# Optimization experiments

Measured on AMD Instinct MI355X. Metric: run time of the kernel, lower is better.

## Reference

```python
import jax, jax.numpy as jnp
import numpy as np

B, S, D = 4, 4096, 2048


def _xavier(key, d):
    bound = (6.0 / (d + d)) ** 0.5
    return jax.random.uniform(key, (d, d), jnp.float32, -bound, bound)


def setup_inputs() -> dict:
    key = jax.random.key(0)
    ks = jax.random.split(key, 7)
    return {
        "x": jax.random.normal(ks[0], (B, S, D), jnp.float32),
        "Wr": _xavier(ks[1], D),
        "Ww": _xavier(ks[2], D),
        "Wk": _xavier(ks[3], D),
        "Wv": _xavier(ks[4], D),
        "Wo": _xavier(ks[5], D),
        "time_decay": jax.random.uniform(ks[6], (D,), jnp.float32, -1.0, 0.0),
    }


def reference(x, Wr, Ww, Wk, Wv, Wo, time_decay):
    # Projections (torch nn.Linear computes x @ W.T)
    r = jax.nn.sigmoid(jnp.einsum("bsd,ed->bse", x, Wr))
    w = -jnp.exp(jnp.einsum("bsd,ed->bse", x, Ww))
    k = jnp.einsum("bsd,ed->bse", x, Wk)
    v = jnp.einsum("bsd,ed->bse", x, Wv)
    ewk = jnp.exp(w + k)                       # [B,S,D]
    decay = jnp.exp(time_decay)                # [D], per-channel decay

    def step(carry, inp):
        num, den = carry                       # each [B,D]
        ewk_t, v_t, r_t = inp                  # each [B,D]
        # t==0 with zero state reduces to ewk*v / ewk, matching torch branch
        num = decay * num + ewk_t * v_t
        den = decay * den + ewk_t
        wkv = num / (den + 1e-8)
        return (num, den), r_t * wkv

    init = (jnp.zeros((B, D), x.dtype), jnp.zeros((B, D), x.dtype))
    xs = (jnp.swapaxes(ewk, 0, 1), jnp.swapaxes(v, 0, 1), jnp.swapaxes(r, 0, 1))
    (num, den), ys = jax.lax.scan(step, init, xs)          # ys: [S,B,D]
    out = jnp.einsum("bsd,ed->bse", jnp.swapaxes(ys, 0, 1), Wo)
    final_state = jnp.stack([num, den], axis=1)            # [B,2,D]
    return out, final_state
```

## Files before the change

kernel.cpp:

```cpp
#include <hip/hip_runtime.h>
#include <cstdint>
#include <cstddef>


typedef unsigned short u16;
typedef __attribute__((ext_vector_type(8))) __bf16 bf16x8;
typedef __attribute__((ext_vector_type(4))) float f32x4;

#define AS1 __attribute__((address_space(1)))
#define AS3 __attribute__((address_space(3)))

static constexpr int BATCH  = 4;
static constexpr int SEQ    = 4096;
static constexpr int DIM    = 2048;
static constexpr int MROWS  = BATCH * SEQ;
static constexpr int NCHUNK = 128;
static constexpr int CLEN   = SEQ / NCHUNK;

__device__ __forceinline__ u16 f2bf(float f) {
    uint32_t u = __float_as_uint(f);
    u += 0x7fffu + ((u >> 16) & 1u);
    return (u16)(u >> 16);
}
__device__ __forceinline__ float bfl(uint32_t w) { return __uint_as_float(w << 16); }
__device__ __forceinline__ float bfh(uint32_t w) { return __uint_as_float(w & 0xffff0000u); }
__device__ __forceinline__ void unpack8(uint4 u, float* f) {
    f[0] = bfl(u.x); f[1] = bfh(u.x); f[2] = bfl(u.y); f[3] = bfh(u.y);
    f[4] = bfl(u.z); f[5] = bfh(u.z); f[6] = bfl(u.w); f[7] = bfh(u.w);
}
__device__ __forceinline__ uint32_t pack2(float a, float b) {
    return (uint32_t)f2bf(a) | ((uint32_t)f2bf(b) << 16);
}

__global__ void __launch_bounds__(256) cvt_kernel(const float* __restrict__ in, u16* __restrict__ out) {
    size_t i = ((size_t)blockIdx.x * blockDim.x + threadIdx.x) * 4;
    float4 f = *(const float4*)(in + i);
    u16 o0 = f2bf(f.x), o1 = f2bf(f.y), o2 = f2bf(f.z), o3 = f2bf(f.w);
    uint2 p = { (uint32_t)o0 | ((uint32_t)o1 << 16), (uint32_t)o2 | ((uint32_t)o3 << 16) };
    *(uint2*)(out + i) = p;
}

template<int EPI>
__global__ void __launch_bounds__(256, 2)
gemm_nt(const u16* __restrict__ A, const u16* __restrict__ Bw,
        float* __restrict__ Cf, u16* __restrict__ Cb) {
    __shared__ __align__(16) u16 As[128 * 32];
    __shared__ __align__(16) u16 Bs[128 * 32];
    const int tid  = threadIdx.x;
    const int lane = tid & 63;
    const int wv   = tid >> 6;
    const int wr   = (wv >> 1) * 64;
    const int wc   = (wv & 1) * 64;
    const int m0   = blockIdx.x * 128;
    const int n0   = blockIdx.y * 128;
    const int fr   = lane & 15;
    const int kg   = (lane >> 4) * 8;
    const int srow = tid >> 2;
    const int skc  = (tid & 3) * 8;

    f32x4 acc[4][4] = {};
    const size_t a_base = (size_t)(m0 + srow) * DIM + skc;
    const size_t b_base = (size_t)(n0 + srow) * DIM + skc;

    for (int k0 = 0; k0 < DIM; k0 += 32) {
        __builtin_amdgcn_global_load_lds((AS1 void*)(A + a_base + k0),
                                         (AS3 void*)(As + tid * 8), 16, 0, 0);
        __builtin_amdgcn_global_load_lds((AS1 void*)(A + a_base + (size_t)64 * DIM + k0),
                                         (AS3 void*)(As + (tid + 256) * 8), 16, 0, 0);
        __builtin_amdgcn_global_load_lds((AS1 void*)(Bw + b_base + k0),
                                         (AS3 void*)(Bs + tid * 8), 16, 0, 0);
        __builtin_amdgcn_global_load_lds((AS1 void*)(Bw + b_base + (size_t)64 * DIM + k0),
                                         (AS3 void*)(Bs + (tid + 256) * 8), 16, 0, 0);
        __syncthreads();
        bf16x8 af[4], bfr[4];
#pragma unroll
        for (int i = 0; i < 4; ++i)
            af[i] = *(const bf16x8*)(As + (wr + i * 16 + fr) * 32 + kg);
#pragma unroll
        for (int j = 0; j < 4; ++j)
            bfr[j] = *(const bf16x8*)(Bs + (wc + j * 16 + fr) * 32 + kg);
#pragma unroll
        for (int i = 0; i < 4; ++i)
#pragma unroll
            for (int j = 0; j < 4; ++j)
                acc[i][j] = __builtin_amdgcn_mfma_f32_16x16x32_bf16(af[i], bfr[j], acc[i][j], 0, 0, 0);
        __syncthreads();
    }

    const int rb_ = (lane >> 4) * 4;
#pragma unroll
    for (int i = 0; i < 4; ++i) {
#pragma unroll
        for (int j = 0; j < 4; ++j) {
#pragma unroll
            for (int rg = 0; rg < 4; ++rg) {
                const int row = m0 + wr + i * 16 + rb_ + rg;
                const int col = n0 + wc + j * 16 + fr;
                const float val = acc[i][j][rg];
                if (EPI == 0) {
                    Cf[(size_t)row * DIM + col] = val;
                } else if (EPI == 1) {
                    Cb[(size_t)row * DIM + col] = f2bf(1.0f / (1.0f + expf(-val)));
                } else {
                    Cb[(size_t)row * DIM + col] = f2bf(val);
                }
            }
        }
    }
}

__global__ void __launch_bounds__(256, 2)
gemm_ewk(const u16* __restrict__ A, const u16* __restrict__ Wk,
         const u16* __restrict__ Ww, u16* __restrict__ E) {
    __shared__ __align__(16) u16 As[128 * 32];
    __shared__ __align__(16) u16 Ks[128 * 32];
    __shared__ __align__(16) u16 Ws[128 * 32];
    const int tid  = threadIdx.x;
    const int lane = tid & 63;
    const int wv   = tid >> 6;
    const int wr   = (wv >> 1) * 64;
    const int wc   = (wv & 1) * 64;
    const int m0   = blockIdx.x * 128;
    const int n0   = blockIdx.y * 128;
    const int fr   = lane & 15;
    const int kg   = (lane >> 4) * 8;
    const int srow = tid >> 2;
    const int skc  = (tid & 3) * 8;

    f32x4 acck[4][4] = {};
    f32x4 accw[4][4] = {};
    const size_t a_base = (size_t)(m0 + srow) * DIM + skc;
    const size_t b_base = (size_t)(n0 + srow) * DIM + skc;

    for (int k0 = 0; k0 < DIM; k0 += 32) {
        __builtin_amdgcn_global_load_lds((AS1 void*)(A + a_base + k0),
                                         (AS3 void*)(As + tid * 8), 16, 0, 0);
        __builtin_amdgcn_global_load_lds((AS1 void*)(A + a_base + (size_t)64 * DIM + k0),
                                         (AS3 void*)(As + (tid + 256) * 8), 16, 0, 0);
        __builtin_amdgcn_global_load_lds((AS1 void*)(Wk + b_base + k0),
                                         (AS3 void*)(Ks + tid * 8), 16, 0, 0);
        __builtin_amdgcn_global_load_lds((AS1 void*)(Wk + b_base + (size_t)64 * DIM + k0),
                                         (AS3 void*)(Ks + (tid + 256) * 8), 16, 0, 0);
        __builtin_amdgcn_global_load_lds((AS1 void*)(Ww + b_base + k0),
                                         (AS3 void*)(Ws + tid * 8), 16, 0, 0);
        __builtin_amdgcn_global_load_lds((AS1 void*)(Ww + b_base + (size_t)64 * DIM + k0),
                                         (AS3 void*)(Ws + (tid + 256) * 8), 16, 0, 0);
        __syncthreads();
        bf16x8 af[4], kf[4], wf[4];
#pragma unroll
        for (int i = 0; i < 4; ++i)
            af[i] = *(const bf16x8*)(As + (wr + i * 16 + fr) * 32 + kg);
#pragma unroll
        for (int j = 0; j < 4; ++j) {
            kf[j] = *(const bf16x8*)(Ks + (wc + j * 16 + fr) * 32 + kg);
            wf[j] = *(const bf16x8*)(Ws + (wc + j * 16 + fr) * 32 + kg);
        }
#pragma unroll
        for (int i = 0; i < 4; ++i)
#pragma unroll
            for (int j = 0; j < 4; ++j) {
                acck[i][j] = __builtin_amdgcn_mfma_f32_16x16x32_bf16(af[i], kf[j], acck[i][j], 0, 0, 0);
                accw[i][j] = __builtin_amdgcn_mfma_f32_16x16x32_bf16(af[i], wf[j], accw[i][j], 0, 0, 0);
            }
        __syncthreads();
    }

    const int rb_ = (lane >> 4) * 4;
#pragma unroll
    for (int i = 0; i < 4; ++i)
#pragma unroll
        for (int j = 0; j < 4; ++j)
#pragma unroll
            for (int rg = 0; rg < 4; ++rg) {
                const int row = m0 + wr + i * 16 + rb_ + rg;
                const int col = n0 + wc + j * 16 + fr;
                const float e = expf(acck[i][j][rg] - expf(accw[i][j][rg]));
                E[(size_t)row * DIM + col] = f2bf(e);
            }
}

__global__ void __launch_bounds__(256)
scan_carry(const u16* __restrict__ ewk, const u16* __restrict__ v,
           const float* __restrict__ td,
           float* __restrict__ carN, float* __restrict__ carD) {
    const int b  = blockIdx.x / NCHUNK;
    const int c  = blockIdx.x % NCHUNK;
    const int d0 = threadIdx.x * 8;
    float dec[8], num[8], den[8];
#pragma unroll
    for (int z = 0; z < 8; ++z) { dec[z] = expf(td[d0 + z]); num[z] = 0.f; den[z] = 0.f; }
    const size_t base = ((size_t)b * SEQ + (size_t)c * CLEN) * DIM + d0;
    for (int t = 0; t < CLEN; ++t) {
        uint4 eu = *(const uint4*)(ewk + base + (size_t)t * DIM);
        uint4 vu = *(const uint4*)(v   + base + (size_t)t * DIM);
        float e[8], vv[8];
        unpack8(eu, e); unpack8(vu, vv);
#pragma unroll
        for (int z = 0; z < 8; ++z) {
            num[z] = dec[z] * num[z] + e[z] * vv[z];
            den[z] = dec[z] * den[z] + e[z];
        }
    }
    const size_t cb = ((size_t)(b * NCHUNK + c)) * DIM + d0;
    *(float4*)(carN + cb)     = { num[0], num[1], num[2], num[3] };
    *(float4*)(carN + cb + 4) = { num[4], num[5], num[6], num[7] };
    *(float4*)(carD + cb)     = { den[0], den[1], den[2], den[3] };
    *(float4*)(carD + cb + 4) = { den[4], den[5], den[6], den[7] };
}

__global__ void __launch_bounds__(256)
scan_combine(const float* __restrict__ carN, const float* __restrict__ carD,
             const float* __restrict__ td,
             float* __restrict__ stN, float* __restrict__ stD,
             float* __restrict__ fs) {
    const int i = blockIdx.x * 256 + threadIdx.x;
    const int b = i >> 11;
    const int d = i & (DIM - 1);
    const float decL = expf(td[d] * (float)CLEN);
    float num = 0.f, den = 0.f;
    for (int c = 0; c < NCHUNK; ++c) {
        const size_t idx = ((size_t)(b * NCHUNK + c)) * DIM + d;
        stN[idx] = num; stD[idx] = den;
        num = decL * num + carN[idx];
        den = decL * den + carD[idx];
    }
    fs[(size_t)b * 2 * DIM + d]       = num;
    fs[(size_t)b * 2 * DIM + DIM + d] = den;
}

__global__ void __launch_bounds__(256)
scan_apply(const u16* __restrict__ ewk, const u16* __restrict__ v,
           const u16* __restrict__ r, const float* __restrict__ td,
           const float* __restrict__ stN, const float* __restrict__ stD,
           u16* __restrict__ y) {
    const int b  = blockIdx.x / NCHUNK;
    const int c  = blockIdx.x % NCHUNK;
    const int d0 = threadIdx.x * 8;
    float dec[8], num[8], den[8];
    const size_t sb = ((size_t)(b * NCHUNK + c)) * DIM + d0;
    {
        float4 n0_ = *(const float4*)(stN + sb), n1_ = *(const float4*)(stN + sb + 4);
        float4 e0_ = *(const float4*)(stD + sb), e1_ = *(const float4*)(stD + sb + 4);
        num[0]=n0_.x; num[1]=n0_.y; num[2]=n0_.z; num[3]=n0_.w;
        num[4]=n1_.x; num[5]=n1_.y; num[6]=n1_.z; num[7]=n1_.w;
        den[0]=e0_.x; den[1]=e0_.y; den[2]=e0_.z; den[3]=e0_.w;
        den[4]=e1_.x; den[5]=e1_.y; den[6]=e1_.z; den[7]=e1_.w;
    }
#pragma unroll
    for (int z = 0; z < 8; ++z) dec[z] = expf(td[d0 + z]);
    const size_t base = ((size_t)b * SEQ + (size_t)c * CLEN) * DIM + d0;
    for (int t = 0; t < CLEN; ++t) {
        uint4 eu = *(const uint4*)(ewk + base + (size_t)t * DIM);
        uint4 vu = *(const uint4*)(v   + base + (size_t)t * DIM);
        uint4 ru = *(const uint4*)(r   + base + (size_t)t * DIM);
        float e[8], vv[8], rr[8], yy[8];
        unpack8(eu, e); unpack8(vu, vv); unpack8(ru, rr);
#pragma unroll
        for (int z = 0; z < 8; ++z) {
            num[z] = dec[z] * num[z] + e[z] * vv[z];
            den[z] = dec[z] * den[z] + e[z];
            yy[z]  = rr[z] * (num[z] / (den[z] + 1e-8f));
        }
        uint4 o = { pack2(yy[0], yy[1]), pack2(yy[2], yy[3]),
                    pack2(yy[4], yy[5]), pack2(yy[6], yy[7]) };
        *(uint4*)(y + base + (size_t)t * DIM) = o;
    }
}

extern "C" void kernel_launch(void* const* d_in, const int* in_sizes, int n_in,
                              void* d_out, int out_size, void* d_ws, size_t ws_size,
                              hipStream_t stream) {
    const float* x  = (const float*)d_in[0];
    const float* Wr = (const float*)d_in[1];
    const float* Ww = (const float*)d_in[2];
    const float* Wk = (const float*)d_in[3];
    const float* Wv = (const float*)d_in[4];
    const float* Wo = (const float*)d_in[5];
    const float* td = (const float*)d_in[6];
    float* out = (float*)d_out;
    float* fs  = out + (size_t)MROWS * DIM;

    uint8_t* w = (uint8_t*)d_ws;
    auto take = [&](size_t bytes) { void* p = (void*)w; w += bytes; return p; };
    u16* xb   = (u16*)take((size_t)MROWS * DIM * 2);
    u16* Wrb  = (u16*)take((size_t)DIM * DIM * 2);
    u16* Wwb  = (u16*)take((size_t)DIM * DIM * 2);
    u16* Wkb  = (u16*)take((size_t)DIM * DIM * 2);
    u16* Wvb  = (u16*)take((size_t)DIM * DIM * 2);
    u16* Wob  = (u16*)take((size_t)DIM * DIM * 2);
    u16* rb   = (u16*)take((size_t)MROWS * DIM * 2);
    u16* vb   = (u16*)take((size_t)MROWS * DIM * 2);
    u16* ewkb = (u16*)take((size_t)MROWS * DIM * 2);
    u16* yb   = (u16*)take((size_t)MROWS * DIM * 2);
    float* carN = (float*)take((size_t)BATCH * NCHUNK * DIM * 4);
    float* carD = (float*)take((size_t)BATCH * NCHUNK * DIM * 4);
    float* stN  = (float*)take((size_t)BATCH * NCHUNK * DIM * 4);
    float* stD  = (float*)take((size_t)BATCH * NCHUNK * DIM * 4);

    cvt_kernel<<<(MROWS * DIM) / 1024, 256, 0, stream>>>(x, xb);
    cvt_kernel<<<(DIM * DIM) / 1024, 256, 0, stream>>>(Wr, Wrb);
    cvt_kernel<<<(DIM * DIM) / 1024, 256, 0, stream>>>(Ww, Wwb);
    cvt_kernel<<<(DIM * DIM) / 1024, 256, 0, stream>>>(Wk, Wkb);
    cvt_kernel<<<(DIM * DIM) / 1024, 256, 0, stream>>>(Wv, Wvb);
    cvt_kernel<<<(DIM * DIM) / 1024, 256, 0, stream>>>(Wo, Wob);

    dim3 gg(MROWS / 128, DIM / 128);
    gemm_nt<1><<<gg, 256, 0, stream>>>(xb, Wrb, nullptr, rb);
    gemm_nt<2><<<gg, 256, 0, stream>>>(xb, Wvb, nullptr, vb);
    gemm_ewk  <<<gg, 256, 0, stream>>>(xb, Wkb, Wwb, ewkb);

    scan_carry  <<<BATCH * NCHUNK, 256, 0, stream>>>(ewkb, vb, td, carN, carD);
    scan_combine<<<(BATCH * DIM) / 256, 256, 0, stream>>>(carN, carD, td, stN, stD, fs);
    scan_apply  <<<BATCH * NCHUNK, 256, 0, stream>>>(ewkb, vb, rb, td, stN, stD, yb);

    gemm_nt<0><<<gg, 256, 0, stream>>>(yb, Wob, out, nullptr);
}
```

Measured before the change: 1.184 ms.

## Fuse conversions, merge r/v GEMMs, and fold scan into one cooperative kernel

Replaces the six conversion launches with a single kernel and merges the r and v projections into one GEMM that shares the A tile across two weight matrices. The three scan kernels become one cooperative kernel with grid-wide syncs between the carry, combine and apply phases. The combine phase now batches its loads over eight chunks. The goal is fewer launches and fewer reads of the x tile, at the cost of more registers in the dual GEMM, which could lower occupancy, plus the overhead of cooperative grid syncs.

```diff
diff --git a/kernel.cpp b/kernel.cpp
--- a/kernel.cpp
+++ b/kernel.cpp
@@ -1,7 +1,10 @@
 #include <hip/hip_runtime.h>
+#include <hip/hip_cooperative_groups.h>
 #include <cstdint>
 #include <cstddef>
 
+
+namespace cg = cooperative_groups;
 
 typedef unsigned short u16;
 typedef __attribute__((ext_vector_type(8))) __bf16 bf16x8;
@@ -32,12 +35,32 @@
     return (uint32_t)f2bf(a) | ((uint32_t)f2bf(b) << 16);
 }
 
-__global__ void __launch_bounds__(256) cvt_kernel(const float* __restrict__ in, u16* __restrict__ out) {
-    size_t i = ((size_t)blockIdx.x * blockDim.x + threadIdx.x) * 4;
-    float4 f = *(const float4*)(in + i);
-    u16 o0 = f2bf(f.x), o1 = f2bf(f.y), o2 = f2bf(f.z), o3 = f2bf(f.w);
-    uint2 p = { (uint32_t)o0 | ((uint32_t)o1 << 16), (uint32_t)o2 | ((uint32_t)o3 << 16) };
-    *(uint2*)(out + i) = p;
+static constexpr int XBLKS = (MROWS * DIM) / 1024;
+static constexpr int WBLKS = (DIM * DIM) / 1024;
+
+__global__ void __launch_bounds__(256)
+cvt_all(const float* __restrict__ x,  const float* __restrict__ Wr,
+        const float* __restrict__ Ww, const float* __restrict__ Wk,
+        const float* __restrict__ Wv, const float* __restrict__ Wo,
+        u16* __restrict__ xb,  u16* __restrict__ Wrb, u16* __restrict__ Wwb,
+        u16* __restrict__ Wkb, u16* __restrict__ Wvb, u16* __restrict__ Wob) {
+    const int blk = blockIdx.x;
+    const float* src;
+    u16* dst;
+    size_t base;
+    if (blk < XBLKS) {
+        src = x; dst = xb; base = (size_t)blk * 1024;
+    } else {
+        const int wsel = (blk - XBLKS) / WBLKS;
+        const int lb   = (blk - XBLKS) % WBLKS;
+        const float* ss[5] = { Wr, Ww, Wk, Wv, Wo };
+        u16*         dd[5] = { Wrb, Wwb, Wkb, Wvb, Wob };
+        src = ss[wsel]; dst = dd[wsel]; base = (size_t)lb * 1024;
+    }
+    const size_t i = base + (size_t)threadIdx.x * 4;
+    float4 f = *(const float4*)(src + i);
+    uint2 p = { pack2(f.x, f.y), pack2(f.z, f.w) };
+    *(uint2*)(dst + i) = p;
 }
 
 template<int EPI>
@@ -179,17 +202,93 @@
             }
 }
 
+__global__ void __launch_bounds__(256, 2)
+gemm_rv(const u16* __restrict__ A, const u16* __restrict__ Wr,
+        const u16* __restrict__ Wv, u16* __restrict__ R, u16* __restrict__ V) {
+    __shared__ __align__(16) u16 As[128 * 32];
+    __shared__ __align__(16) u16 Rs[128 * 32];
+    __shared__ __align__(16) u16 Vs[128 * 32];
+    const int tid  = threadIdx.x;
+    const int lane = tid & 63;
+    const int wv   = tid >> 6;
+    const int wr   = (wv >> 1) * 64;
+    const int wc   = (wv & 1) * 64;
+    const int m0   = blockIdx.x * 128;
+    const int n0   = blockIdx.y * 128;
+    const int fr   = lane & 15;
+    const int kg   = (lane >> 4) * 8;
+    const int srow = tid >> 2;
+    const int skc  = (tid & 3) * 8;
+
+    f32x4 accr[4][4] = {};
+    f32x4 accv[4][4] = {};
+    const size_t a_base = (size_t)(m0 + srow) * DIM + skc;
+    const size_t b_base = (size_t)(n0 + srow) * DIM + skc;
+
+    for (int k0 = 0; k0 < DIM; k0 += 32) {
+        __builtin_amdgcn_global_load_lds((AS1 void*)(A + a_base + k0),
+                                         (AS3 void*)(As + tid * 8), 16, 0, 0);
+        __builtin_amdgcn_global_load_lds((AS1 void*)(A + a_base + (size_t)64 * DIM + k0),
+                                         (AS3 void*)(As + (tid + 256) * 8), 16, 0, 0);
+        __builtin_amdgcn_global_load_lds((AS1 void*)(Wr + b_base + k0),
+                                         (AS3 void*)(Rs + tid * 8), 16, 0, 0);
+        __builtin_amdgcn_global_load_lds((AS1 void*)(Wr + b_base + (size_t)64 * DIM + k0),
+                                         (AS3 void*)(Rs + (tid + 256) * 8), 16, 0, 0);
+        __builtin_amdgcn_global_load_lds((AS1 void*)(Wv + b_base + k0),
+                                         (AS3 void*)(Vs + tid * 8), 16, 0, 0);
+        __builtin_amdgcn_global_load_lds((AS1 void*)(Wv + b_base + (size_t)64 * DIM + k0),
+                                         (AS3 void*)(Vs + (tid + 256) * 8), 16, 0, 0);
+        __syncthreads();
+        bf16x8 af[4], rf[4], vf[4];
+#pragma unroll
+        for (int i = 0; i < 4; ++i)
+            af[i] = *(const bf16x8*)(As + (wr + i * 16 + fr) * 32 + kg);
+#pragma unroll
+        for (int j = 0; j < 4; ++j) {
+            rf[j] = *(const bf16x8*)(Rs + (wc + j * 16 + fr) * 32 + kg);
+            vf[j] = *(const bf16x8*)(Vs + (wc + j * 16 + fr) * 32 + kg);
+        }
+#pragma unroll
+        for (int i = 0; i < 4; ++i)
+#pragma unroll
+            for (int j = 0; j < 4; ++j) {
+                accr[i][j] = __builtin_amdgcn_mfma_f32_16x16x32_bf16(af[i], rf[j], accr[i][j], 0, 0, 0);
+                accv[i][j] = __builtin_amdgcn_mfma_f32_16x16x32_bf16(af[i], vf[j], accv[i][j], 0, 0, 0);
+            }
+        __syncthreads();
+    }
+
+    const int rb_ = (lane >> 4) * 4;
+#pragma unroll
+    for (int i = 0; i < 4; ++i)
+#pragma unroll
+        for (int j = 0; j < 4; ++j)
+#pragma unroll
+            for (int rg = 0; rg < 4; ++rg) {
+                const int row = m0 + wr + i * 16 + rb_ + rg;
+                const int col = n0 + wc + j * 16 + fr;
+                R[(size_t)row * DIM + col] = f2bf(1.0f / (1.0f + expf(-accr[i][j][rg])));
+                V[(size_t)row * DIM + col] = f2bf(accv[i][j][rg]);
+            }
+}
+
 __global__ void __launch_bounds__(256)
-scan_carry(const u16* __restrict__ ewk, const u16* __restrict__ v,
-           const float* __restrict__ td,
-           float* __restrict__ carN, float* __restrict__ carD) {
+scan_coop(const u16* __restrict__ ewk, const u16* __restrict__ v,
+          const u16* __restrict__ r, const float* __restrict__ td,
+          float* __restrict__ carN, float* __restrict__ carD,
+          float* __restrict__ stN, float* __restrict__ stD,
+          float* __restrict__ fs, u16* __restrict__ y) {
+    cg::grid_group grid = cg::this_grid();
     const int b  = blockIdx.x / NCHUNK;
     const int c  = blockIdx.x % NCHUNK;
     const int d0 = threadIdx.x * 8;
+    const size_t base = ((size_t)b * SEQ + (size_t)c * CLEN) * DIM + d0;
+    const size_t cb   = ((size_t)(b * NCHUNK + c)) * DIM + d0;
+
     float dec[8], num[8], den[8];
 #pragma unroll
     for (int z = 0; z < 8; ++z) { dec[z] = expf(td[d0 + z]); num[z] = 0.f; den[z] = 0.f; }
-    const size_t base = ((size_t)b * SEQ + (size_t)c * CLEN) * DIM + d0;
+
     for (int t = 0; t < CLEN; ++t) {
         uint4 eu = *(const uint4*)(ewk + base + (size_t)t * DIM);
         uint4 vu = *(const uint4*)(v   + base + (size_t)t * DIM);
@@ -201,54 +300,48 @@
             den[z] = dec[z] * den[z] + e[z];
         }
     }
-    const size_t cb = ((size_t)(b * NCHUNK + c)) * DIM + d0;
     *(float4*)(carN + cb)     = { num[0], num[1], num[2], num[3] };
     *(float4*)(carN + cb + 4) = { num[4], num[5], num[6], num[7] };
     *(float4*)(carD + cb)     = { den[0], den[1], den[2], den[3] };
     *(float4*)(carD + cb + 4) = { den[4], den[5], den[6], den[7] };
-}
-
-__global__ void __launch_bounds__(256)
-scan_combine(const float* __restrict__ carN, const float* __restrict__ carD,
-             const float* __restrict__ td,
-             float* __restrict__ stN, float* __restrict__ stD,
-             float* __restrict__ fs) {
-    const int i = blockIdx.x * 256 + threadIdx.x;
-    const int b = i >> 11;
-    const int d = i & (DIM - 1);
-    const float decL = expf(td[d] * (float)CLEN);
-    float num = 0.f, den = 0.f;
-    for (int c = 0; c < NCHUNK; ++c) {
-        const size_t idx = ((size_t)(b * NCHUNK + c)) * DIM + d;
-        stN[idx] = num; stD[idx] = den;
-        num = decL * num + carN[idx];
-        den = decL * den + carD[idx];
-    }
-    fs[(size_t)b * 2 * DIM + d]       = num;
-    fs[(size_t)b * 2 * DIM + DIM + d] = den;
-}
-
-__global__ void __launch_bounds__(256)
-scan_apply(const u16* __restrict__ ewk, const u16* __restrict__ v,
-           const u16* __restrict__ r, const float* __restrict__ td,
-           const float* __restrict__ stN, const float* __restrict__ stD,
-           u16* __restrict__ y) {
-    const int b  = blockIdx.x / NCHUNK;
-    const int c  = blockIdx.x % NCHUNK;
-    const int d0 = threadIdx.x * 8;
-    float dec[8], num[8], den[8];
-    const size_t sb = ((size_t)(b * NCHUNK + c)) * DIM + d0;
+
+    grid.sync();
+
+    const size_t gt = (size_t)blockIdx.x * 256 + threadIdx.x;
+    if (gt < (size_t)BATCH * DIM) {
+        const int bb = (int)(gt >> 11);
+        const int d  = (int)(gt & (DIM - 1));
+        const float decL = expf(td[d] * (float)CLEN);
+        float n2 = 0.f, d2 = 0.f;
+        for (int cc = 0; cc < NCHUNK; cc += 8) {
+            float cn[8], cd[8];
+#pragma unroll
+            for (int u = 0; u < 8; ++u) {
+                const size_t idx = ((size_t)(bb * NCHUNK + cc + u)) * DIM + d;
+                cn[u] = carN[idx]; cd[u] = carD[idx];
+            }
+#pragma unroll
+            for (int u = 0; u < 8; ++u) {
+                const size_t idx = ((size_t)(bb * NCHUNK + cc + u)) * DIM + d;
+                stN[idx] = n2; stD[idx] = d2;
+                n2 = decL * n2 + cn[u];
+                d2 = decL * d2 + cd[u];
+            }
+        }
+        fs[(size_t)bb * 2 * DIM + d]       = n2;
+        fs[(size_t)bb * 2 * DIM + DIM + d] = d2;
+    }
+
+    grid.sync();
+
     {
-        float4 n0_ = *(const float4*)(stN + sb), n1_ = *(const float4*)(stN + sb + 4);
-        float4 e0_ = *(const float4*)(stD + sb), e1_ = *(const float4*)(stD + sb + 4);
+        float4 n0_ = *(const float4*)(stN + cb), n1_ = *(const float4*)(stN + cb + 4);
+        float4 e0_ = *(const float4*)(stD + cb), e1_ = *(const float4*)(stD + cb + 4);
         num[0]=n0_.x; num[1]=n0_.y; num[2]=n0_.z; num[3]=n0_.w;
         num[4]=n1_.x; num[5]=n1_.y; num[6]=n1_.z; num[7]=n1_.w;
         den[0]=e0_.x; den[1]=e0_.y; den[2]=e0_.z; den[3]=e0_.w;
         den[4]=e1_.x; den[5]=e1_.y; den[6]=e1_.z; den[7]=e1_.w;
     }
-#pragma unroll
-    for (int z = 0; z < 8; ++z) dec[z] = expf(td[d0 + z]);
-    const size_t base = ((size_t)b * SEQ + (size_t)c * CLEN) * DIM + d0;
     for (int t = 0; t < CLEN; ++t) {
         uint4 eu = *(const uint4*)(ewk + base + (size_t)t * DIM);
         uint4 vu = *(const uint4*)(v   + base + (size_t)t * DIM);
@@ -297,21 +390,21 @@
     float* stN  = (float*)take((size_t)BATCH * NCHUNK * DIM * 4);
     float* stD  = (float*)take((size_t)BATCH * NCHUNK * DIM * 4);
 
-    cvt_kernel<<<(MROWS * DIM) / 1024, 256, 0, stream>>>(x, xb);
-    cvt_kernel<<<(DIM * DIM) / 1024, 256, 0, stream>>>(Wr, Wrb);
-    cvt_kernel<<<(DIM * DIM) / 1024, 256, 0, stream>>>(Ww, Wwb);
-    cvt_kernel<<<(DIM * DIM) / 1024, 256, 0, stream>>>(Wk, Wkb);
-    cvt_kernel<<<(DIM * DIM) / 1024, 256, 0, stream>>>(Wv, Wvb);
-    cvt_kernel<<<(DIM * DIM) / 1024, 256, 0, stream>>>(Wo, Wob);
+    cvt_all<<<XBLKS + 5 * WBLKS, 256, 0, stream>>>(x, Wr, Ww, Wk, Wv, Wo,
+                                                   xb, Wrb, Wwb, Wkb, Wvb, Wob);
 
     dim3 gg(MROWS / 128, DIM / 128);
-    gemm_nt<1><<<gg, 256, 0, stream>>>(xb, Wrb, nullptr, rb);
-    gemm_nt<2><<<gg, 256, 0, stream>>>(xb, Wvb, nullptr, vb);
-    gemm_ewk  <<<gg, 256, 0, stream>>>(xb, Wkb, Wwb, ewkb);
-
-    scan_carry  <<<BATCH * NCHUNK, 256, 0, stream>>>(ewkb, vb, td, carN, carD);
-    scan_combine<<<(BATCH * DIM) / 256, 256, 0, stream>>>(carN, carD, td, stN, stD, fs);
-    scan_apply  <<<BATCH * NCHUNK, 256, 0, stream>>>(ewkb, vb, rb, td, stN, stD, yb);
+    gemm_rv <<<gg, 256, 0, stream>>>(xb, Wrb, Wvb, rb, vb);
+    gemm_ewk<<<gg, 256, 0, stream>>>(xb, Wkb, Wwb, ewkb);
+
+    {
+        void* args[] = { (void*)&ewkb, (void*)&vb, (void*)&rb, (void*)&td,
+                         (void*)&carN, (void*)&carD, (void*)&stN, (void*)&stD,
+                         (void*)&fs, (void*)&yb };
+        hipLaunchCooperativeKernel((const void*)scan_coop,
+                                   dim3(BATCH * NCHUNK), dim3(256),
+                                   args, 0, stream);
+    }
 
     gemm_nt<0><<<gg, 256, 0, stream>>>(yb, Wob, out, nullptr);
 }
```

Result: slower. 1.266 ms (+6.9%).
